# Optimization experiments

Hardware: AMD Instinct MI355X
Metric: run time of the kernel (lower is better)

Reference implementation:

```python
import jax, jax.numpy as jnp
import numpy as np

IN_DIM = 128
MEM_DIM = 256
NUM_CLASSES = 12
NUM_LEVELS = 17  # complete binary tree, N = 2**17 - 1 = 131071 nodes


def setup_inputs() -> dict:
    key = jax.random.key(0)
    ks = jax.random.split(key, 7)
    N = 2 ** NUM_LEVELS - 1
    s = 1.0 / np.sqrt(MEM_DIM)  # PyTorch LSTMCell/Linear init scale
    return {
        "x": jax.random.normal(ks[0], (N, IN_DIM), dtype=jnp.float32),
        "W_ih": jax.random.uniform(ks[1], (4 * MEM_DIM, IN_DIM), jnp.float32, -s, s),
        "b_ih": jax.random.uniform(ks[2], (4 * MEM_DIM,), jnp.float32, -s, s),
        "W_hh": jax.random.uniform(ks[3], (4 * MEM_DIM, MEM_DIM), jnp.float32, -s, s),
        "b_hh": jax.random.uniform(ks[4], (4 * MEM_DIM,), jnp.float32, -s, s),
        "W_fc": jax.random.uniform(ks[5], (NUM_CLASSES, MEM_DIM), jnp.float32, -s, s),
        "b_fc": jax.random.uniform(ks[6], (NUM_CLASSES,), jnp.float32, -s, s),
        "num_levels": NUM_LEVELS,
    }


def reference(x, W_ih, b_ih, W_hh, b_hh, W_fc, b_fc, num_levels):
    # Complete binary tree in BFS order: level l occupies nodes [2^l-1, 2^(l+1)-2];
    # children of level-l nodes are exactly the (contiguous) level-(l+1) nodes.
    mem = W_hh.shape[1]
    h_below = None
    c_below = None
    for l in reversed(range(num_levels)):
        n = 2 ** l
        x_l = x[n - 1:2 * n - 1]  # [n, in_dim] nodes at this level
        if h_below is None:  # leaves: zero child state
            ch_h = jnp.zeros((n, mem), dtype=x.dtype)
            ch_c = ch_h
        else:  # sum the two children's (h, c), as the recursion accumulates
            ch_h = h_below.reshape(n, 2, mem).sum(axis=1)
            ch_c = c_below.reshape(n, 2, mem).sum(axis=1)
        # PyTorch LSTMCell: gates = x W_ih^T + b_ih + h W_hh^T + b_hh, chunks i,f,g,o
        gates = x_l @ W_ih.T + b_ih + ch_h @ W_hh.T + b_hh  # [n, 4*mem]
        i, f, g, o = jnp.split(gates, 4, axis=-1)
        c_new = jax.nn.sigmoid(f) * ch_c + jax.nn.sigmoid(i) * jnp.tanh(g)
        h_new = jax.nn.sigmoid(o) * jnp.tanh(c_new)
        h_below, c_below = h_new, c_new
    # Original applies FC to state[1] == cell state c of the root (kept faithfully).
    return c_below[:1] @ W_fc.T + b_fc  # [1, num_classes]
```

## Files before the change

### kernel.cpp

```cpp
#include <hip/hip_runtime.h>
#include <hip/hip_bf16.h>
#include <cstddef>

#define IN_DIM 128
#define MEM 256
#define KTOT 384
#define NLEAF 65536
#define NBLK_TAIL 8

typedef float f32x4 __attribute__((ext_vector_type(4)));
typedef short s16x8 __attribute__((ext_vector_type(8)));
typedef unsigned int u32;

__device__ inline unsigned short f2bf(float f){
    unsigned int u = __builtin_bit_cast(unsigned int, f);
    u += 0x7fff + ((u >> 16) & 1);
    return (unsigned short)(u >> 16);
}

__device__ inline void gld_lds16(const void* g, void* l){
    __builtin_amdgcn_global_load_lds((const __attribute__((address_space(1))) u32*)g,
                                     (__attribute__((address_space(3))) u32*)l, 16, 0, 0);
}
__device__ inline void gld_lds16_dev(const void* g, void* l){
    __builtin_amdgcn_global_load_lds((const __attribute__((address_space(1))) u32*)g,
                                     (__attribute__((address_space(3))) u32*)l, 16, 0, 17);
}
__device__ inline void st16_dev(unsigned short* p, unsigned short v){
    unsigned int vv = v;
    asm volatile("global_store_short %0, %1, off sc0 sc1" :: "v"(p), "v"(vv) : "memory");
}
__device__ inline void st32_dev(float* p, float v){
    asm volatile("global_store_dword %0, %1, off sc0 sc1" :: "v"(p), "v"(v) : "memory");
}

__device__ inline float fsigm(float x){
    return __builtin_amdgcn_rcpf(1.f + __expf(-x));
}
__device__ inline float ftanh(float x){
    return 2.f * __builtin_amdgcn_rcpf(1.f + __expf(-2.f * x)) - 1.f;
}

__host__ __device__ inline size_t offA(int l){
    if (l == 16) return 0;
    return 8388608u + 384u * (65536u - (1u << (l + 1)));
}
#define ARENA_ELEMS 33554048u
#define ARENA_PAD   65536u

__device__ inline void grid_barrier_nf(unsigned* ctr, unsigned target){
    asm volatile("s_waitcnt vmcnt(0)" ::: "memory");
    __syncthreads();
    if (threadIdx.x == 0){
        __hip_atomic_fetch_add(ctr, 1u, __ATOMIC_RELAXED, __HIP_MEMORY_SCOPE_AGENT);
        while (__hip_atomic_load(ctr, __ATOMIC_RELAXED, __HIP_MEMORY_SCOPE_AGENT) < target)
            __builtin_amdgcn_s_sleep(2);
    }
    __syncthreads();
}

__global__ void pack_kernel(const float* __restrict__ x,
                            const float* __restrict__ W_ih, const float* __restrict__ b_ih,
                            const float* __restrict__ W_hh, const float* __restrict__ b_hh,
                            unsigned short* __restrict__ Wp, float* __restrict__ bp,
                            unsigned short* __restrict__ Aarena, unsigned* __restrict__ ctr){
    const int stride = gridDim.x * blockDim.x;
    const int tid0 = blockIdx.x * blockDim.x + threadIdx.x;
    if (tid0 == 0){ ctr[0] = 0; }

    for (int g = tid0; g < 1024 * 48; g += stride){
        int row = g / 48, ko = (g - row * 48) * 8;
        const float* s = (ko < IN_DIM) ? (W_ih + (size_t)row * IN_DIM + ko)
                                       : (W_hh + (size_t)row * MEM + (ko - IN_DIM));
        f32x4 v0 = *(const f32x4*)s, v1 = *(const f32x4*)(s + 4);
        s16x8 o;
        #pragma unroll
        for (int e = 0; e < 4; ++e){ o[e] = (short)f2bf(v0[e]); o[4+e] = (short)f2bf(v1[e]); }
        *(s16x8*)(Wp + (size_t)row * KTOT + ko) = o;
        if (ko == 0) bp[row] = b_ih[row] + b_hh[row];
    }

    const int TOTAL_G = 131071 * 16;
    for (int g = tid0; g < TOTAL_G; g += stride){
        int i  = g >> 4;
        int ko = (g & 15) * 8;
        int l  = 31 - __clz(i + 1);
        int j  = i + 1 - (1 << l);
        size_t dst = offA(l) + (size_t)j * ((l == 16) ? 128 : 384) + ko;
        const f32x4* s = (const f32x4*)(x + (size_t)i * IN_DIM + ko);
        f32x4 v0 = s[0], v1 = s[1];
        s16x8 o;
        #pragma unroll
        for (int e = 0; e < 4; ++e){ o[e] = (short)f2bf(v0[e]); o[4+e] = (short)f2bf(v1[e]); }
        *(s16x8*)(Aarena + dst) = o;
    }
}

template<int NK>
__global__ __launch_bounds__(512, 1) void gemm_lstm8p_kernel(
    const unsigned short* __restrict__ A, int n,
    const unsigned short* __restrict__ Wp, const float* __restrict__ bp,
    const float* __restrict__ csum_in,
    unsigned short* __restrict__ A_next, float* __restrict__ csum_out)
{
    __shared__ __align__(16) unsigned short As[2][2][128 * 64];
    __shared__ __align__(16) unsigned short Bs[2][2][128 * 64];

    const int tid  = threadIdx.x;
    const int lane = tid & 63;
    const int wid  = tid >> 6;
    const int wm   = wid >> 2;
    const int wn   = wid & 3;
    const int row0 = blockIdx.x * 256;
    const int m0   = blockIdx.y * 64;
    const int mg   = m0 + wn * 16 + (lane & 15);

    auto stageA = [&](int kt, int h){
        #pragma unroll
        for (int i = 0; i < 2; ++i){
            int p  = i * 512 + tid;
            int r  = p >> 3;
            int ls = (p & 7) ^ (r & 7);
            gld_lds16(A + (size_t)(row0 + h * 128 + r) * NK + kt * 64 + ls * 8,
                      (char*)As[kt & 1][h] + (size_t)(i * 512 + wid * 64) * 16);
        }
    };
    auto stageB = [&](int kt, int h){
        #pragma unroll
        for (int i = 0; i < 2; ++i){
            int p  = i * 512 + tid;
            int r  = p >> 3;
            int b  = h * 128 + r;
            int grow = (b >> 6) * 256 + m0 + (b & 63);
            int ls = (p & 7) ^ (r & 7);
            gld_lds16(Wp + (size_t)grow * KTOT + kt * 64 + ls * 8,
                      (char*)Bs[kt & 1][h] + (size_t)(i * 512 + wid * 64) * 16);
        }
    };

    f32x4 acc[8][4];
    #pragma unroll
    for (int r = 0; r < 8; ++r)
        #pragma unroll
        for (int q = 0; q < 4; ++q)
            acc[r][q] = (f32x4){0.f, 0.f, 0.f, 0.f};

    constexpr int nkt = NK / 64;
    stageA(0, 0); stageA(0, 1); stageB(0, 0);
    if (nkt > 1) stageB(1, 0);
    stageB(0, 1);

    s16x8 bfr[2][2];

    #pragma unroll
    for (int t = 0; t < nkt; ++t){
        const unsigned short* Ab = As[t & 1][wm];
        const unsigned short* Bb0 = Bs[t & 1][0];
        const unsigned short* Bb1 = Bs[t & 1][1];

        if (t + 1 < nkt) { asm volatile("s_waitcnt vmcnt(4)" ::: "memory"); }
        else             { asm volatile("s_waitcnt vmcnt(2)" ::: "memory"); }
        __builtin_amdgcn_s_barrier();
        asm volatile("" ::: "memory");

        #pragma unroll
        for (int rh = 0; rh < 2; ++rh){
            s16x8 a[4][2];
            #pragma unroll
            for (int j = 0; j < 4; ++j)
                #pragma unroll
                for (int ks = 0; ks < 2; ++ks){
                    int kb = (((ks * 4 + (lane >> 4)) ^ (lane & 7))) * 8;
                    a[j][ks] = *(const s16x8*)(Ab + (size_t)(rh * 64 + j * 16 + (lane & 15)) * 64 + kb);
                }
            if (rh == 0){
                #pragma unroll
                for (int q2 = 0; q2 < 2; ++q2)
                    #pragma unroll
                    for (int ks = 0; ks < 2; ++ks){
                        int kb = (((ks * 4 + (lane >> 4)) ^ (lane & 7))) * 8;
                        bfr[q2][ks] = *(const s16x8*)(Bb0 + (size_t)(q2 * 64 + wn * 16 + (lane & 15)) * 64 + kb);
                    }
                if (t + 1 < nkt) stageA(t + 1, 0);
            } else {
                if (t + 1 < nkt) stageA(t + 1, 1);
            }
            __builtin_amdgcn_s_setprio(1);
            #pragma unroll
            for (int j = 0; j < 4; ++j)
                #pragma unroll
                for (int q2 = 0; q2 < 2; ++q2)
                    #pragma unroll
                    for (int ks = 0; ks < 2; ++ks)
                        acc[rh * 4 + j][q2] = __builtin_amdgcn_mfma_f32_16x16x32_bf16(
                            a[j][ks], bfr[q2][ks], acc[rh * 4 + j][q2], 0, 0, 0);
            __builtin_amdgcn_s_setprio(0);
        }

        if (t + 1 < nkt) { asm volatile("s_waitcnt vmcnt(4)" ::: "memory"); }
        else             { asm volatile("s_waitcnt vmcnt(0)" ::: "memory"); }
        __builtin_amdgcn_s_barrier();
        asm volatile("" ::: "memory");

        #pragma unroll
        for (int rh = 0; rh < 2; ++rh){
            s16x8 a[4][2];
            #pragma unroll
            for (int j = 0; j < 4; ++j)
                #pragma unroll
                for (int ks = 0; ks < 2; ++ks){
                    int kb = (((ks * 4 + (lane >> 4)) ^ (lane & 7))) * 8;
                    a[j][ks] = *(const s16x8*)(Ab + (size_t)(rh * 64 + j * 16 + (lane & 15)) * 64 + kb);
                }
            if (rh == 0){
                #pragma unroll
                for (int q2 = 0; q2 < 2; ++q2)
                    #pragma unroll
                    for (int ks = 0; ks < 2; ++ks){
                        int kb = (((ks * 4 + (lane >> 4)) ^ (lane & 7))) * 8;
                        bfr[q2][ks] = *(const s16x8*)(Bb1 + (size_t)(q2 * 64 + wn * 16 + (lane & 15)) * 64 + kb);
                    }
                if (t + 2 < nkt) stageB(t + 2, 0);
            } else {
                if (t + 1 < nkt) stageB(t + 1, 1);
            }
            __builtin_amdgcn_s_setprio(1);
            #pragma unroll
            for (int j = 0; j < 4; ++j)
                #pragma unroll
                for (int q2 = 0; q2 < 2; ++q2)
                    #pragma unroll
                    for (int ks = 0; ks < 2; ++ks)
                        acc[rh * 4 + j][2 + q2] = __builtin_amdgcn_mfma_f32_16x16x32_bf16(
                            a[j][ks], bfr[q2][ks], acc[rh * 4 + j][2 + q2], 0, 0, 0);
            __builtin_amdgcn_s_setprio(0);
        }
        __builtin_amdgcn_s_barrier();
        asm volatile("" ::: "memory");
    }

    const float b0 = bp[0 * 256 + mg];
    const float b1 = bp[1 * 256 + mg];
    const float b2 = bp[2 * 256 + mg];
    const float b3 = bp[3 * 256 + mg];
    #pragma unroll
    for (int r = 0; r < 8; ++r){
        const int base = row0 + wm * 128 + r * 16 + (lane >> 4) * 4;
        float cpre[4];
        #pragma unroll
        for (int e = 0; e < 4; ++e)
            cpre[e] = csum_in[(size_t)(base + e) * MEM + mg];
        float cn[4], hn[4];
        #pragma unroll
        for (int e = 0; e < 4; ++e){
            float iv = acc[r][0][e] + b0;
            float fv = acc[r][1][e] + b1;
            float gv = acc[r][2][e] + b2;
            float ov = acc[r][3][e] + b3;
            float c  = fsigm(fv) * cpre[e] + fsigm(iv) * ftanh(gv);
            cn[e] = c;
            hn[e] = fsigm(ov) * ftanh(c);
        }
        int p0 = base >> 1;
        A_next[(size_t)p0 * KTOT + IN_DIM + mg] = f2bf(hn[0] + hn[1]);
        csum_out[(size_t)p0 * MEM + mg] = cn[0] + cn[1];
        A_next[(size_t)(p0 + 1) * KTOT + IN_DIM + mg] = f2bf(hn[2] + hn[3]);
        csum_out[(size_t)(p0 + 1) * MEM + mg] = cn[2] + cn[3];
    }
}

#define KC 64

template<int NK, int RB, bool LEAF>
__global__ __launch_bounds__(256) void gemm_lstm_kernel(
    const unsigned short* __restrict__ A, int n,
    const unsigned short* __restrict__ Wp, const float* __restrict__ bp,
    const float* __restrict__ csum_in,
    unsigned short* __restrict__ A_next, float* __restrict__ csum_out)
{
    constexpr int BM = RB * 32;
    __shared__ __align__(16) unsigned short As[2][BM * KC];
    __shared__ __align__(16) unsigned short Bs[2][128 * KC];

    const int tid  = threadIdx.x;
    const int lane = tid & 63;
    const int wid  = tid >> 6;
    const int wm   = wid >> 1;
    const int wc   = wid & 1;
    const int row0 = blockIdx.x * BM;
    const int m0   = blockIdx.y * 32;

    const int srow = lane >> 3;
    const int scol = ((lane & 7) ^ srow) * 8;

    const int mg = m0 + wc * 16 + (lane & 15);

    const float b0 = bp[0 * 256 + mg];
    const float b1 = LEAF ? 0.f : bp[1 * 256 + mg];
    const float b2 = bp[2 * 256 + mg];
    const float b3 = bp[3 * 256 + mg];
    float cpre[RB][4];
    if (!LEAF){
        #pragma unroll
        for (int r = 0; r < RB; ++r){
            const int base = row0 + wm * (RB * 16) + r * 16 + (lane >> 4) * 4;
            #pragma unroll
            for (int e = 0; e < 4; ++e)
                cpre[r][e] = csum_in[(size_t)(base + e) * MEM + mg];
        }
    }

    f32x4 acc[RB][4];
    #pragma unroll
    for (int r = 0; r < RB; ++r)
        #pragma unroll
        for (int q = 0; q < 4; ++q)
            acc[r][q] = (f32x4){0.f, 0.f, 0.f, 0.f};

    auto stage = [&](int d, int kk){
        char* asb = (char*)As[d];
        char* bsb = (char*)Bs[d];
        #pragma unroll
        for (int q = 0; q < RB; ++q){
            int t = wid * RB + q;
            int r = t * 8 + srow;
            gld_lds16(A + (size_t)(row0 + r) * NK + kk + scol, asb + t * 1024);
        }
        #pragma unroll
        for (int q = 0; q < 4; ++q){
            int t = wid * 4 + q;
            int b = t * 8 + srow;
            int grow = (b >> 5) * 256 + m0 + (b & 31);
            gld_lds16(Wp + (size_t)grow * KTOT + kk + scol, bsb + t * 1024);
        }
    };

    constexpr int nIter = NK / KC;
    stage(0, 0);
    int buf = 0;
    #pragma unroll
    for (int it = 0; it < nIter; ++it){
        if (it + 1 < nIter){
            stage(buf ^ 1, (it + 1) * KC);
            if constexpr (RB == 4) asm volatile("s_waitcnt vmcnt(8)" ::: "memory");
            else                   asm volatile("s_waitcnt vmcnt(6)" ::: "memory");
        } else {
            asm volatile("s_waitcnt vmcnt(0)" ::: "memory");
        }
        __builtin_amdgcn_s_barrier();
        const unsigned short* Ab = As[buf];
        const unsigned short* Bb = Bs[buf];
        #pragma unroll
        for (int ks = 0; ks < 2; ++ks){
            const int slot = ks * 4 + (lane >> 4);
            const int kb = (slot ^ (lane & 7)) * 8;
            s16x8 a[RB], b[4];
            #pragma unroll
            for (int r = 0; r < RB; ++r)
                a[r] = *(const s16x8*)(Ab + (wm * (RB * 16) + r * 16 + (lane & 15)) * KC + kb);
            #pragma unroll
            for (int q = 0; q < 4; ++q)
                b[q] = *(const s16x8*)(Bb + (q * 32 + wc * 16 + (lane & 15)) * KC + kb);
            #pragma unroll
            for (int r = 0; r < RB; ++r)
                #pragma unroll
                for (int q = 0; q < 4; ++q)
                    acc[r][q] = __builtin_amdgcn_mfma_f32_16x16x32_bf16(a[r], b[q], acc[r][q], 0, 0, 0);
        }
        __builtin_amdgcn_s_barrier();
        buf ^= 1;
    }

    #pragma unroll
    for (int r = 0; r < RB; ++r){
        const int base = row0 + wm * (RB * 16) + r * 16 + (lane >> 4) * 4;
        float cn[4], hn[4];
        #pragma unroll
        for (int e = 0; e < 4; ++e){
            float iv = acc[r][0][e] + b0;
            float gv = acc[r][2][e] + b2;
            float ov = acc[r][3][e] + b3;
            float c;
            if (LEAF){
                c = fsigm(iv) * ftanh(gv);
            } else {
                float fv = acc[r][1][e] + b1;
                c = fsigm(fv) * cpre[r][e] + fsigm(iv) * ftanh(gv);
            }
            cn[e] = c;
            hn[e] = fsigm(ov) * ftanh(c);
        }
        if (base < n){
            int p0 = base >> 1;
            A_next[(size_t)p0 * KTOT + IN_DIM + mg] = f2bf(hn[0] + hn[1]);
            csum_out[(size_t)p0 * MEM + mg] = cn[0] + cn[1];
        }
        if (base + 2 < n){
            int p1 = (base >> 1) + 1;
            A_next[(size_t)p1 * KTOT + IN_DIM + mg] = f2bf(hn[2] + hn[3]);
            csum_out[(size_t)p1 * MEM + mg] = cn[2] + cn[3];
        }
    }
}

__global__ __launch_bounds__(512) void tail_kernel(
    const unsigned short* __restrict__ arena,
    const unsigned short* __restrict__ Wp, const float* __restrict__ bp,
    float* cs_in, float* cs_out,
    float* __restrict__ c_root,
    const float* __restrict__ W_fc, const float* __restrict__ b_fc,
    float* __restrict__ out, unsigned* __restrict__ ctr)
{
    __shared__ __align__(16) unsigned short WpL[128 * KTOT];
    __shared__ __align__(16) unsigned short AL[64 * KTOT];

    const int tid  = threadIdx.x;
    const int lane = tid & 63;
    const int wid  = tid >> 6;
    const int wm   = wid >> 1;
    const int wc   = wid & 1;
    const int m0   = blockIdx.x * 32;
    const int mg   = m0 + wc * 16 + (lane & 15);

    #pragma unroll
    for (int i = 0; i < 12; ++i){
        int p0 = wid * 768 + i * 64;
        int p  = p0 + lane;
        int lrow  = p / 48;
        int pslot = p % 48;
        int lslot = pslot ^ (lrow & 7);
        int grow  = (lrow >> 5) * 256 + m0 + (lrow & 31);
        gld_lds16(Wp + (size_t)grow * KTOT + lslot * 8, (char*)WpL + (size_t)p0 * 16);
    }

    const float b0 = bp[0 * 256 + mg];
    const float b1 = bp[1 * 256 + mg];
    const float b2 = bp[2 * 256 + mg];
    const float b3 = bp[3 * 256 + mg];

    asm volatile("s_waitcnt vmcnt(0)" ::: "memory");
    __builtin_amdgcn_s_barrier();

    unsigned gen = 0;
    for (int l = 7; l >= 0; --l){
        const int n = 1 << l;
        const unsigned short* Al = arena + offA(l);
        const int nhalf = (n > 64) ? (n >> 6) : 1;

        for (int h = 0; h < nhalf; ++h){
            const int r0 = h * 64;
            const int rows = (n < 64) ? n : 64;

            const int nslots = rows * 48;
            for (int t = 0; t * 512 < nslots; ++t){
                int pbase = t * 512 + wid * 64;
                int p = pbase + lane;
                if (p < nslots){
                    int row   = p / 48;
                    int pslot = p - row * 48;
                    int lslot = pslot ^ (row & 7);
                    gld_lds16_dev(Al + (size_t)(r0 + row) * KTOT + lslot * 8,
                                  (char*)AL + (size_t)pbase * 16);
                }
            }

            const int base = r0 + wm * 16 + (lane >> 4) * 4;
            float cpre[4];
            #pragma unroll
            for (int e = 0; e < 4; ++e)
                cpre[e] = __hip_atomic_load(&cs_in[(size_t)(base + e) * MEM + mg],
                                            __ATOMIC_RELAXED, __HIP_MEMORY_SCOPE_AGENT);

            asm volatile("s_waitcnt vmcnt(0)" ::: "memory");
            __builtin_amdgcn_s_barrier();

            f32x4 acc[4];
            #pragma unroll
            for (int q = 0; q < 4; ++q)
                acc[q] = (f32x4){0.f, 0.f, 0.f, 0.f};

            #pragma unroll
            for (int kc = 0; kc < 12; ++kc){
                const int ls = kc * 4 + (lane >> 4);
                const int kb = (ls ^ (lane & 7)) * 8;
                s16x8 a = *(const s16x8*)(AL + (size_t)(wm * 16 + (lane & 15)) * KTOT + kb);
                s16x8 b[4];
                #pragma unroll
                for (int q = 0; q < 4; ++q)
                    b[q] = *(const s16x8*)(WpL + (q * 32 + wc * 16 + (lane & 15)) * KTOT + kb);
                #pragma unroll
                for (int q = 0; q < 4; ++q)
                    acc[q] = __builtin_amdgcn_mfma_f32_16x16x32_bf16(a, b[q], acc[q], 0, 0, 0);
            }

            {
                float cn[4], hn[4];
                #pragma unroll
                for (int e = 0; e < 4; ++e){
                    float iv = acc[0][e] + b0;
                    float fv = acc[1][e] + b1;
                    float gv = acc[2][e] + b2;
                    float ov = acc[3][e] + b3;
                    float c  = fsigm(fv) * cpre[e] + fsigm(iv) * ftanh(gv);
                    cn[e] = c;
                    hn[e] = fsigm(ov) * ftanh(c);
                }
                if (l == 0){
                    if (base == 0) st32_dev(&c_root[mg], cn[0]);
                } else {
                    unsigned short* A_next = (unsigned short*)arena + offA(l - 1);
                    if (base < n){
                        int p0 = base >> 1;
                        st16_dev(&A_next[(size_t)p0 * KTOT + IN_DIM + mg], f2bf(hn[0] + hn[1]));
                        st32_dev(&cs_out[(size_t)p0 * MEM + mg], cn[0] + cn[1]);
                    }
                    if (base + 2 < n){
                        int p1 = (base >> 1) + 1;
                        st16_dev(&A_next[(size_t)p1 * KTOT + IN_DIM + mg], f2bf(hn[2] + hn[3]));
                        st32_dev(&cs_out[(size_t)p1 * MEM + mg], cn[2] + cn[3]);
                    }
                }
            }
            __builtin_amdgcn_s_barrier();
        }

        float* t = cs_in; cs_in = cs_out; cs_out = t;
        ++gen;
        grid_barrier_nf(ctr, (unsigned)(NBLK_TAIL * gen));
    }

    if (blockIdx.x == 0 && wid < 4){
        int w = wid;
        for (int cls = w * 3; cls < w * 3 + 3; ++cls){
            float s = 0.f;
            for (int m = lane; m < 256; m += 64){
                float cr = __hip_atomic_load(&c_root[m], __ATOMIC_RELAXED, __HIP_MEMORY_SCOPE_AGENT);
                s += cr * W_fc[cls * 256 + m];
            }
            #pragma unroll
            for (int off = 32; off; off >>= 1)
                s += __shfl_down(s, off, 64);
            if (lane == 0) out[cls] = s + b_fc[cls];
        }
    }
}

extern "C" void kernel_launch(void* const* d_in, const int* in_sizes, int n_in,
                              void* d_out, int out_size, void* d_ws, size_t ws_size,
                              hipStream_t stream)
{
    const float* x    = (const float*)d_in[0];
    const float* W_ih = (const float*)d_in[1];
    const float* b_ih = (const float*)d_in[2];
    const float* W_hh = (const float*)d_in[3];
    const float* b_hh = (const float*)d_in[4];
    const float* W_fc = (const float*)d_in[5];
    const float* b_fc = (const float*)d_in[6];
    float* out = (float*)d_out;

    const size_t OFF_WP = 0;
    const size_t OFF_BP = 786432;
    const size_t OFF_A  = 790528;
    const size_t OFF_CS0 = OFF_A + (size_t)(ARENA_ELEMS + ARENA_PAD) * 2;
    const size_t OFF_CS1 = OFF_CS0 + 33554432;
    const size_t OFF_CR  = OFF_CS1 + 33554432;
    const size_t OFF_CTR = OFF_CR + 1024;
    const size_t NEEDED  = OFF_CTR + 64;
    if (ws_size < NEEDED) return;

    char* ws = (char*)d_ws;
    unsigned short* Wp    = (unsigned short*)(ws + OFF_WP);
    float* bp             = (float*)(ws + OFF_BP);
    unsigned short* arena = (unsigned short*)(ws + OFF_A);
    float* cs0            = (float*)(ws + OFF_CS0);
    float* cs1            = (float*)(ws + OFF_CS1);
    float* c_root         = (float*)(ws + OFF_CR);
    unsigned* ctr         = (unsigned*)(ws + OFF_CTR);

    pack_kernel<<<dim3(2048), dim3(256), 0, stream>>>(
        x, W_ih, b_ih, W_hh, b_hh, Wp, bp, arena, ctr);

    gemm_lstm_kernel<IN_DIM, 2, true><<<dim3(NLEAF / 64, 8), dim3(256), 0, stream>>>(
        arena + offA(16), NLEAF, Wp, bp,
        nullptr, arena + offA(15), cs0);

    gemm_lstm8p_kernel<KTOT><<<dim3(128, 4), dim3(512), 0, stream>>>(
        arena + offA(15), 32768, Wp, bp, cs0, arena + offA(14), cs1);
    gemm_lstm8p_kernel<KTOT><<<dim3(64, 4), dim3(512), 0, stream>>>(
        arena + offA(14), 16384, Wp, bp, cs1, arena + offA(13), cs0);

    gemm_lstm_kernel<KTOT, 4, false><<<dim3(64, 8), dim3(256), 0, stream>>>(
        arena + offA(13), 8192, Wp, bp, cs0, arena + offA(12), cs1);

    float* cs_in = cs1; float* cs_out = cs0;
    for (int l = 12; l >= 8; --l){
        int n = 1 << l;
        gemm_lstm_kernel<KTOT, 2, false><<<dim3(n / 64, 8), dim3(256), 0, stream>>>(
            arena + offA(l), n, Wp, bp,
            cs_in, arena + offA(l - 1), cs_out);
        float* t = cs_in; cs_in = cs_out; cs_out = t;
    }

    tail_kernel<<<dim3(NBLK_TAIL), dim3(512), 0, stream>>>(
        arena, Wp, bp, cs_in, cs_out, c_root, W_fc, b_fc, out, ctr);
}
```

Measured before the change: 193.9 us.

## Move non-leaf x packing into leaf GEMM kernel and enlarge leaf tile

The pack kernel now converts only the leaf-level x rows to bf16. Packing of the internal-node x rows moves into the tail of the leaf GEMM/LSTM kernel, so it overlaps with leaf compute instead of sitting serially before it. The leaf kernel's row tile also grows from 64 to 128 rows (RB 2 to 4), halving its block count. The trade-off is extra memory traffic and work inside the leaf kernel, plus fewer blocks there.

After: 193.3 us. About the same (-0.3%).

```diff
diff --git a/kernel.cpp b/kernel.cpp
--- a/kernel.cpp
+++ b/kernel.cpp
@@ -80,19 +80,16 @@
         if (ko == 0) bp[row] = b_ih[row] + b_hh[row];
     }
 
-    const int TOTAL_G = 131071 * 16;
+    const int TOTAL_G = 65536 * 16;
     for (int g = tid0; g < TOTAL_G; g += stride){
-        int i  = g >> 4;
+        int j  = g >> 4;
         int ko = (g & 15) * 8;
-        int l  = 31 - __clz(i + 1);
-        int j  = i + 1 - (1 << l);
-        size_t dst = offA(l) + (size_t)j * ((l == 16) ? 128 : 384) + ko;
-        const f32x4* s = (const f32x4*)(x + (size_t)i * IN_DIM + ko);
+        const f32x4* s = (const f32x4*)(x + (size_t)(65535 + j) * IN_DIM + ko);
         f32x4 v0 = s[0], v1 = s[1];
         s16x8 o;
         #pragma unroll
         for (int e = 0; e < 4; ++e){ o[e] = (short)f2bf(v0[e]); o[4+e] = (short)f2bf(v1[e]); }
-        *(s16x8*)(Aarena + dst) = o;
+        *(s16x8*)(Aarena + (size_t)j * IN_DIM + ko) = o;
     }
 }
 
@@ -271,12 +268,13 @@
 
 #define KC 64
 
-template<int NK, int RB, bool LEAF>
+template<int NK, int RB, bool LEAF, bool PACKX>
 __global__ __launch_bounds__(256) void gemm_lstm_kernel(
     const unsigned short* __restrict__ A, int n,
     const unsigned short* __restrict__ Wp, const float* __restrict__ bp,
     const float* __restrict__ csum_in,
-    unsigned short* __restrict__ A_next, float* __restrict__ csum_out)
+    unsigned short* __restrict__ A_next, float* __restrict__ csum_out,
+    const float* __restrict__ xsrc, unsigned short* __restrict__ arena)
 {
     constexpr int BM = RB * 32;
     __shared__ __align__(16) unsigned short As[2][BM * KC];
@@ -399,6 +397,25 @@
             int p1 = (base >> 1) + 1;
             A_next[(size_t)p1 * KTOT + IN_DIM + mg] = f2bf(hn[2] + hn[3]);
             csum_out[(size_t)p1 * MEM + mg] = cn[2] + cn[3];
+        }
+    }
+
+    if constexpr (PACKX){
+        const int TG = 65535 * 16;
+        const int bid = blockIdx.y * gridDim.x + blockIdx.x;
+        const int stride_g = gridDim.x * gridDim.y * 256;
+        for (int g = bid * 256 + tid; g < TG; g += stride_g){
+            int i  = g >> 4;
+            int ko = (g & 15) * 8;
+            int l  = 31 - __clz(i + 1);
+            int j  = i + 1 - (1 << l);
+            size_t dst = offA(l) + (size_t)j * KTOT + ko;
+            const f32x4* s = (const f32x4*)(xsrc + (size_t)i * IN_DIM + ko);
+            f32x4 v0 = s[0], v1 = s[1];
+            s16x8 o;
+            #pragma unroll
+            for (int e = 0; e < 4; ++e){ o[e] = (short)f2bf(v0[e]); o[4+e] = (short)f2bf(v1[e]); }
+            *(s16x8*)(arena + dst) = o;
         }
     }
 }
@@ -580,24 +597,24 @@
     pack_kernel<<<dim3(2048), dim3(256), 0, stream>>>(
         x, W_ih, b_ih, W_hh, b_hh, Wp, bp, arena, ctr);
 
-    gemm_lstm_kernel<IN_DIM, 2, true><<<dim3(NLEAF / 64, 8), dim3(256), 0, stream>>>(
+    gemm_lstm_kernel<IN_DIM, 4, true, true><<<dim3(NLEAF / 128, 8), dim3(256), 0, stream>>>(
         arena + offA(16), NLEAF, Wp, bp,
-        nullptr, arena + offA(15), cs0);
+        nullptr, arena + offA(15), cs0, x, arena);
 
     gemm_lstm8p_kernel<KTOT><<<dim3(128, 4), dim3(512), 0, stream>>>(
         arena + offA(15), 32768, Wp, bp, cs0, arena + offA(14), cs1);
     gemm_lstm8p_kernel<KTOT><<<dim3(64, 4), dim3(512), 0, stream>>>(
         arena + offA(14), 16384, Wp, bp, cs1, arena + offA(13), cs0);
 
-    gemm_lstm_kernel<KTOT, 4, false><<<dim3(64, 8), dim3(256), 0, stream>>>(
-        arena + offA(13), 8192, Wp, bp, cs0, arena + offA(12), cs1);
+    gemm_lstm_kernel<KTOT, 4, false, false><<<dim3(64, 8), dim3(256), 0, stream>>>(
+        arena + offA(13), 8192, Wp, bp, cs0, arena + offA(12), cs1, nullptr, nullptr);
 
     float* cs_in = cs1; float* cs_out = cs0;
     for (int l = 12; l >= 8; --l){
         int n = 1 << l;
-        gemm_lstm_kernel<KTOT, 2, false><<<dim3(n / 64, 8), dim3(256), 0, stream>>>(
+        gemm_lstm_kernel<KTOT, 2, false, false><<<dim3(n / 64, 8), dim3(256), 0, stream>>>(
             arena + offA(l), n, Wp, bp,
-            cs_in, arena + offA(l - 1), cs_out);
+            cs_in, arena + offA(l - 1), cs_out, nullptr, nullptr);
         float* t = cs_in; cs_in = cs_out; cs_out = t;
     }
 
```
